# Kernel optimization log

Hardware: AMD Instinct MI355X
Metric: run time of the kernel (lower is better)

Reference implementation:

```python
import jax, jax.numpy as jnp
import numpy as np

B, T, E = 2, 2048, 1024
H, D = 16, 64          # num_heads, head_dim (v_head_dim == head_dim)


def setup_inputs() -> dict:
    key = jax.random.key(0)
    ks = jax.random.split(key, 10)
    s = lambda fan_in: 1.0 / np.sqrt(fan_in)
    inp = {
        "embed": jax.random.normal(ks[0], (B, T, E), dtype=jnp.float32),
        "mask": jax.random.randint(ks[1], (B, T, T), 0, 2) > 0,
        # Linear weights stored as [in, out] (y = x @ W + b)
        "Wq": jax.random.uniform(ks[2], (E, H * D), minval=-s(E), maxval=s(E)),
        "bq": jnp.zeros((H * D,), jnp.float32),
        "Wk": jax.random.uniform(ks[3], (E, H * D), minval=-s(E), maxval=s(E)),
        "bk": jnp.zeros((H * D,), jnp.float32),
        "Wv": jax.random.uniform(ks[4], (E, H * D), minval=-s(E), maxval=s(E)),
        "bv": jnp.zeros((H * D,), jnp.float32),
        "Wz": jax.random.uniform(ks[5], (H * D, E), minval=-s(H * D), maxval=s(H * D)),
        "bz": jnp.zeros((E,), jnp.float32),
    }
    return inp


def reference(embed, mask, Wq, bq, Wk, bk, Wv, bv, Wz, bz):
    # Self-attention: context = embed
    q = (embed @ Wq + bq).reshape(B, T, H, D)   # b t h d
    k = (embed @ Wk + bk).reshape(B, T, H, D)   # b T h d
    v = (embed @ Wv + bv).reshape(B, T, H, D)   # b T h d

    scale = D ** (-0.5)
    score = jnp.einsum('bthd,bThd->bhtT', q, k) * scale   # [b,h,t,T] materialized, as in source
    max_neg = -jnp.finfo(score.dtype).max
    score = jnp.where(mask[:, None, :, :], score, max_neg)
    norm_score = jax.nn.softmax(score, axis=-1)
    z = jnp.einsum('bhtT,bThd->bthd', norm_score, v)      # [b,t,h,d]
    flat_z = z.reshape(B, T, H * D)
    return flat_z @ Wz + bz
```

## Files before the change

### kernel.cpp

```cpp
#include <hip/hip_runtime.h>
#include <hip/hip_bf16.h>


typedef __bf16 bf8_t  __attribute__((ext_vector_type(8)));
typedef __bf16 bf4_t  __attribute__((ext_vector_type(4)));
typedef float  f4_t   __attribute__((ext_vector_type(4)));

constexpr int Bb = 2, Tt = 2048, Hh = 16, Dd = 64;

#define ASYNC16(g, l)                                                        \
    __builtin_amdgcn_global_load_lds(                                        \
        (const __attribute__((address_space(1))) void*)(g),                  \
        (__attribute__((address_space(3))) void*)(l), 16, 0, 0)

#if __has_builtin(__builtin_amdgcn_exp2f)
#define EXP2F(x) __builtin_amdgcn_exp2f(x)
#else
#define EXP2F(x) exp2f(x)
#endif

__global__ __launch_bounds__(256) void prep_kernel(
    const float* __restrict__ embed, const int* __restrict__ mask,
    const float* __restrict__ w0, const float* __restrict__ w1,
    const float* __restrict__ w2, const float* __restrict__ w3,
    __bf16* __restrict__ o0, __bf16* __restrict__ o1,
    __bf16* __restrict__ o2, __bf16* __restrict__ o3,
    __bf16* __restrict__ Eb, unsigned* __restrict__ Mbits)
{
    int z = blockIdx.x;
    if (z < 4096) {
        const float* in; __bf16* out;
        switch (z >> 10) {
            case 0: in = w0; out = o0; break;
            case 1: in = w1; out = o1; break;
            case 2: in = w2; out = o2; break;
            default: in = w3; out = o3; break;
        }
        int rem = z & 1023;
        int bx = (rem & 31) * 32;
        int by = (rem >> 5) * 32;
        __shared__ float t[32][33];
        int x  = threadIdx.x & 31;
        int y0 = threadIdx.x >> 5;
        #pragma unroll
        for (int i = 0; i < 4; i++) {
            int y = y0 + i * 8;
            t[y][x] = in[(size_t)(by + y) * 1024 + bx + x];
        }
        __syncthreads();
        #pragma unroll
        for (int i = 0; i < 4; i++) {
            int y = y0 + i * 8;
            out[(size_t)(bx + y) * 1024 + by + x] = (__bf16)t[x][y];
        }
    } else if (z < 5120) {
        size_t base = (size_t)(z - 4096) * 4096;
        #pragma unroll
        for (int j = 0; j < 4; j++) {
            size_t i = base + j * 1024 + threadIdx.x * 4;
            float4 v = *reinterpret_cast<const float4*>(embed + i);
            bf4_t o = {(__bf16)v.x, (__bf16)v.y, (__bf16)v.z, (__bf16)v.w};
            *reinterpret_cast<bf4_t*>(Eb + i) = o;
        }
    } else {
        size_t g = (size_t)(z - 5120) * 256 + threadIdx.x;
        const int* mp = mask + g * 32;
        unsigned v = 0;
        #pragma unroll
        for (int i = 0; i < 8; i++) {
            int4 m4 = *reinterpret_cast<const int4*>(mp + i * 4);
            if (m4.x) v |= 1u << (i * 4 + 0);
            if (m4.y) v |= 1u << (i * 4 + 1);
            if (m4.z) v |= 1u << (i * 4 + 2);
            if (m4.w) v |= 1u << (i * 4 + 3);
        }
        Mbits[g] = v;
    }
}

template <int TM, typename OutT>
__device__ __forceinline__ void gemm_body(const __bf16* __restrict__ A,
                                          const __bf16* __restrict__ Bt,
                                          const float* __restrict__ bias,
                                          OutT* __restrict__ out,
                                          int mode, float oscale, int bx, int by)
{
    constexpr int NI = TM / 32;
    alignas(16) __shared__ __bf16 As[TM * 64];
    alignas(16) __shared__ __bf16 Bs[128 * 64];

    int tid  = threadIdx.x;
    int lane = tid & 63;
    int quad = lane >> 4;
    int l16  = lane & 15;
    int wave = tid >> 6;
    int wm   = wave >> 1, wn = wave & 1;

    f4_t acc[NI][4];
    #pragma unroll
    for (int i = 0; i < NI; i++)
        #pragma unroll
        for (int j = 0; j < 4; j++)
            acc[i][j] = f4_t{0.f, 0.f, 0.f, 0.f};

    for (int kt = 0; kt < 1024; kt += 64) {
        #pragma unroll
        for (int i = 0; i < TM / 32; i++) {
            int c   = tid + 256 * i;
            int row = c >> 3, j = c & 7;
            ASYNC16(A + (size_t)(by * TM + row) * 1024 + kt + ((j ^ (row & 7)) * 8),
                    &As[c * 8]);
        }
        #pragma unroll
        for (int i = 0; i < 4; i++) {
            int c   = tid + 256 * i;
            int row = c >> 3, j = c & 7;
            ASYNC16(Bt + (size_t)(bx * 128 + row) * 1024 + kt + ((j ^ (row & 7)) * 8),
                    &Bs[c * 8]);
        }
        __syncthreads();

        bf8_t af[2][NI], bfr[2][4];
        #pragma unroll
        for (int c = 0; c < 2; c++) {
            #pragma unroll
            for (int im = 0; im < NI; im++) {
                int row = wm * (TM / 2) + im * 16 + l16;
                af[c][im] = *reinterpret_cast<const bf8_t*>(
                    &As[row * 64 + (((c * 4 + quad) ^ (row & 7)) * 8)]);
            }
            #pragma unroll
            for (int in_ = 0; in_ < 4; in_++) {
                int row = wn * 64 + in_ * 16 + l16;
                bfr[c][in_] = *reinterpret_cast<const bf8_t*>(
                    &Bs[row * 64 + (((c * 4 + quad) ^ (row & 7)) * 8)]);
            }
        }
        #pragma unroll
        for (int c = 0; c < 2; c++)
            #pragma unroll
            for (int im = 0; im < NI; im++)
                #pragma unroll
                for (int in_ = 0; in_ < 4; in_++)
                    acc[im][in_] = __builtin_amdgcn_mfma_f32_16x16x32_bf16(
                        af[c][im], bfr[c][in_], acc[im][in_], 0, 0, 0);
        __syncthreads();
    }

    #pragma unroll
    for (int im = 0; im < NI; im++) {
        #pragma unroll
        for (int in_ = 0; in_ < 4; in_++) {
            int gc  = bx * 128 + wn * 64 + in_ * 16 + l16;
            float bb = bias[gc];
            int gr0 = by * TM + wm * (TM / 2) + im * 16 + quad * 4;
            if (mode == 2) {
                int b = gr0 >> 11, t0 = gr0 & 2047;
                int h = gc >> 6,  d = gc & 63;
                bf4_t ov;
                #pragma unroll
                for (int r = 0; r < 4; r++)
                    ov[r] = (__bf16)(acc[im][in_][r] + bb);
                *reinterpret_cast<bf4_t*>(
                    (__bf16*)out + ((size_t)(b * Hh + h) * Dd + d) * Tt + t0) = ov;
            } else {
                #pragma unroll
                for (int r = 0; r < 4; r++) {
                    int gr  = gr0 + r;
                    float v = (acc[im][in_][r] + bb) * oscale;
                    size_t idx;
                    if (mode == 0) {
                        idx = (size_t)gr * 1024 + gc;
                    } else {
                        int b = gr >> 11, t = gr & 2047;
                        int h = gc >> 6,  d = gc & 63;
                        idx = ((size_t)(b * Hh + h) * Tt + t) * Dd + d;
                    }
                    out[idx] = (OutT)v;
                }
            }
        }
    }
}

__global__ __launch_bounds__(256) void gemm_qkv_kernel(
    const __bf16* __restrict__ A,
    const __bf16* __restrict__ WqT, const __bf16* __restrict__ WkT, const __bf16* __restrict__ WvT,
    const float* __restrict__ bq,  const float* __restrict__ bk,  const float* __restrict__ bv,
    __bf16* __restrict__ Qo, __bf16* __restrict__ Ko, __bf16* __restrict__ Vo)
{
    const __bf16* Bt; const float* bias; __bf16* out; int mode; float sc;
    if      (blockIdx.z == 0) { Bt = WqT; bias = bq; out = Qo; mode = 1; sc = 0.18033688011112042f; }
    else if (blockIdx.z == 1) { Bt = WkT; bias = bk; out = Ko; mode = 1; sc = 1.f; }
    else                      { Bt = WvT; bias = bv; out = Vo; mode = 2; sc = 1.f; }
    gemm_body<128, __bf16>(A, Bt, bias, out, mode, sc, blockIdx.x, blockIdx.y);
}

__global__ __launch_bounds__(256) void gemm_out_kernel(
    const __bf16* __restrict__ A, const __bf16* __restrict__ Bt,
    const float* __restrict__ bias, float* __restrict__ out)
{
    gemm_body<64, float>(A, Bt, bias, out, 0, 1.f, blockIdx.x, blockIdx.y);
}

__global__ __launch_bounds__(512, 4) void flash_kernel(
    const __bf16* __restrict__ Qb, const __bf16* __restrict__ Kb,
    const __bf16* __restrict__ Vb, const unsigned* __restrict__ Mbits,
    __bf16* __restrict__ Zb)
{
    alignas(16) __shared__ __bf16 Ks[2][64 * 64];
    alignas(16) __shared__ __bf16 Vs[2][64 * 64];
    alignas(16) __shared__ __bf16 Ps[8 * 16 * 72];

    int tid  = threadIdx.x;
    int lane = tid & 63;
    int wave = tid >> 6;
    int quad = lane >> 4;
    int l16  = lane & 15;
    int b = blockIdx.z, h = blockIdx.y;
    int bh = b * Hh + h;
    int qrow = blockIdx.x * 128 + wave * 16;

    int srow = tid >> 3, sj = tid & 7;
    const __bf16* kgp = Kb + ((size_t)bh * Tt + srow) * Dd + ((sj ^ (srow & 7)) * 8);
    const __bf16* vgp = Vb + ((size_t)bh * Dd + srow) * Tt + ((sj ^ (srow & 7)) * 8);
    const int sdst = tid * 8;

    bf8_t qf[2];
    #pragma unroll
    for (int c = 0; c < 2; c++)
        qf[c] = *reinterpret_cast<const bf8_t*>(
            Qb + ((size_t)bh * Tt + qrow + l16) * Dd + c * 32 + quad * 8);

    bf8_t ones;
    #pragma unroll
    for (int i = 0; i < 8; i++) ones[i] = (__bf16)1.0f;

    const unsigned* bmp = Mbits + ((size_t)b * Tt + qrow + l16) * 64;

    f4_t lacc = f4_t{0.f, 0.f, 0.f, 0.f};
    f4_t o[4];
    #pragma unroll
    for (int d = 0; d < 4; d++) o[d] = f4_t{0.f, 0.f, 0.f, 0.f};

    __bf16* pw = Ps + wave * 16 * 72;

    bf8_t kreg = *reinterpret_cast<const bf8_t*>(kgp);
    bf8_t vreg = *reinterpret_cast<const bf8_t*>(vgp);
    unsigned long long mreg = *reinterpret_cast<const unsigned long long*>(bmp);

    for (int kt = 0; kt < Tt; kt += 64) {
        int par = (kt >> 6) & 1;
        *reinterpret_cast<bf8_t*>(&Ks[par][sdst]) = kreg;
        *reinterpret_cast<bf8_t*>(&Vs[par][sdst]) = vreg;
        unsigned nib[4];
        #pragma unroll
        for (int n = 0; n < 4; n++)
            nib[n] = (unsigned)(mreg >> (n * 16 + quad * 4)) & 0xFu;
        __syncthreads();

        int ktn = (kt + 64 < Tt) ? kt + 64 : 0;
        kreg = *reinterpret_cast<const bf8_t*>(kgp + (size_t)ktn * Dd);
        vreg = *reinterpret_cast<const bf8_t*>(vgp + ktn);
        mreg = *reinterpret_cast<const unsigned long long*>(bmp + (ktn >> 5));

        f4_t s[4];
        #pragma unroll
        for (int n = 0; n < 4; n++) s[n] = f4_t{0.f, 0.f, 0.f, 0.f};
        __builtin_amdgcn_s_setprio(1);
        #pragma unroll
        for (int c = 0; c < 2; c++)
            #pragma unroll
            for (int n = 0; n < 4; n++) {
                int krow = n * 16 + l16;
                bf8_t kf = *reinterpret_cast<const bf8_t*>(
                    &Ks[par][krow * 64 + (((c * 4 + quad) ^ (krow & 7)) * 8)]);
                s[n] = __builtin_amdgcn_mfma_f32_16x16x32_bf16(kf, qf[c], s[n], 0, 0, 0);
            }
        __builtin_amdgcn_s_setprio(0);

        #pragma unroll
        for (int n = 0; n < 4; n++) {
            bf4_t pv4;
            #pragma unroll
            for (int r = 0; r < 4; r++) {
                float p = (nib[n] & (1u << r)) ? EXP2F(s[n][r]) : 0.f;
                pv4[r] = (__bf16)p;
            }
            *reinterpret_cast<bf4_t*>(&pw[l16 * 72 + n * 16 + quad * 4]) = pv4;
        }

        __builtin_amdgcn_s_setprio(1);
        #pragma unroll
        for (int c = 0; c < 2; c++) {
            bf8_t pf = *reinterpret_cast<const bf8_t*>(
                &pw[l16 * 72 + c * 32 + quad * 8]);
            lacc = __builtin_amdgcn_mfma_f32_16x16x32_bf16(ones, pf, lacc, 0, 0, 0);
            #pragma unroll
            for (int ds = 0; ds < 4; ds++) {
                int vrow = ds * 16 + l16;
                bf8_t vf = *reinterpret_cast<const bf8_t*>(
                    &Vs[par][vrow * 64 + (((c * 4 + quad) ^ (vrow & 7)) * 8)]);
                o[ds] = __builtin_amdgcn_mfma_f32_16x16x32_bf16(vf, pf, o[ds], 0, 0, 0);
            }
        }
        __builtin_amdgcn_s_setprio(0);
    }

    float inv = 1.f / fmaxf(lacc[0], 1e-30f);
    size_t zrow = ((size_t)b * Tt + qrow + l16) * 1024 + h * 64;
    #pragma unroll
    for (int ds = 0; ds < 4; ds++) {
        bf4_t ov;
        #pragma unroll
        for (int r = 0; r < 4; r++) ov[r] = (__bf16)(o[ds][r] * inv);
        *reinterpret_cast<bf4_t*>(Zb + zrow + ds * 16 + quad * 4) = ov;
    }
}

extern "C" void kernel_launch(void* const* d_in, const int* in_sizes, int n_in,
                              void* d_out, int out_size, void* d_ws, size_t ws_size,
                              hipStream_t stream)
{
    (void)in_sizes; (void)n_in; (void)out_size; (void)ws_size;

    const float* embed = (const float*)d_in[0];
    const int*   mask  = (const int*)d_in[1];
    const float* Wq = (const float*)d_in[2];
    const float* bq = (const float*)d_in[3];
    const float* Wk = (const float*)d_in[4];
    const float* bk = (const float*)d_in[5];
    const float* Wv = (const float*)d_in[6];
    const float* bv = (const float*)d_in[7];
    const float* Wz = (const float*)d_in[8];
    const float* bz = (const float*)d_in[9];
    float* out = (float*)d_out;

    char* ws = (char*)d_ws;
    const size_t MB = (size_t)1024 * 1024;
    __bf16*   WqT = (__bf16*)(ws + 0 * MB);
    __bf16*   WkT = (__bf16*)(ws + 2 * MB);
    __bf16*   WvT = (__bf16*)(ws + 4 * MB);
    __bf16*   WzT = (__bf16*)(ws + 6 * MB);
    __bf16*   Eb  = (__bf16*)(ws + 8 * MB);
    __bf16*   Qb  = (__bf16*)(ws + 16 * MB);
    __bf16*   Kb  = (__bf16*)(ws + 24 * MB);
    __bf16*   Vb  = (__bf16*)(ws + 32 * MB);
    __bf16*   Zb  = (__bf16*)(ws + 40 * MB);
    unsigned* Mb  = (unsigned*)(ws + 48 * MB);

    prep_kernel<<<dim3(6144), 256, 0, stream>>>(embed, mask, Wq, Wk, Wv, Wz,
                                                WqT, WkT, WvT, WzT, Eb, Mb);
    gemm_qkv_kernel<<<dim3(8, 32, 3), 256, 0, stream>>>(Eb, WqT, WkT, WvT,
                                                        bq, bk, bv, Qb, Kb, Vb);
    flash_kernel<<<dim3(16, Hh, Bb), 512, 0, stream>>>(Qb, Kb, Vb, Mb, Zb);
    gemm_out_kernel<<<dim3(8, 64, 1), 256, 0, stream>>>(Zb, WzT, bz, out);
}
```

Before: 224.2 us.

## Split each flash query tile's key block across two waves with final reduction

```diff
diff --git a/kernel.cpp b/kernel.cpp
--- a/kernel.cpp
+++ b/kernel.cpp
@@ -203,28 +203,35 @@
     gemm_body<64, float>(A, Bt, bias, out, 0, 1.f, blockIdx.x, blockIdx.y);
 }
 
-__global__ __launch_bounds__(512, 4) void flash_kernel(
+__global__ __launch_bounds__(1024, 8) void flash_kernel(
     const __bf16* __restrict__ Qb, const __bf16* __restrict__ Kb,
     const __bf16* __restrict__ Vb, const unsigned* __restrict__ Mbits,
     __bf16* __restrict__ Zb)
 {
-    alignas(16) __shared__ __bf16 Ks[2][64 * 64];
-    alignas(16) __shared__ __bf16 Vs[2][64 * 64];
-    alignas(16) __shared__ __bf16 Ps[8 * 16 * 72];
+    alignas(16) __shared__ char smem[51200];
+    __bf16* Ks = (__bf16*)smem;
+    __bf16* Vs = (__bf16*)(smem + 16384);
+    __bf16* Ps = (__bf16*)(smem + 32768);
+    float*  fscr = (float*)smem;
 
     int tid  = threadIdx.x;
     int lane = tid & 63;
     int wave = tid >> 6;
+    int s    = wave >> 1;
+    int hk   = wave & 1;
     int quad = lane >> 4;
     int l16  = lane & 15;
     int b = blockIdx.z, h = blockIdx.y;
     int bh = b * Hh + h;
-    int qrow = blockIdx.x * 128 + wave * 16;
-
-    int srow = tid >> 3, sj = tid & 7;
+    int qrow = blockIdx.x * 128 + s * 16;
+
+    int st = tid & 511, srow = st >> 3, sj = st & 7;
+    bool stageK = (wave < 8);
     const __bf16* kgp = Kb + ((size_t)bh * Tt + srow) * Dd + ((sj ^ (srow & 7)) * 8);
     const __bf16* vgp = Vb + ((size_t)bh * Dd + srow) * Tt + ((sj ^ (srow & 7)) * 8);
-    const int sdst = tid * 8;
+    const __bf16* sgp = stageK ? kgp : vgp;
+    const size_t  sstep = stageK ? (size_t)64 * Dd : (size_t)64;
+    __bf16* sdstp = (stageK ? Ks : Vs) + st * 8;
 
     bf8_t qf[2];
     #pragma unroll
@@ -243,78 +250,93 @@
     #pragma unroll
     for (int d = 0; d < 4; d++) o[d] = f4_t{0.f, 0.f, 0.f, 0.f};
 
-    __bf16* pw = Ps + wave * 16 * 72;
-
-    bf8_t kreg = *reinterpret_cast<const bf8_t*>(kgp);
-    bf8_t vreg = *reinterpret_cast<const bf8_t*>(vgp);
+    __bf16* pw = Ps + s * (16 * 72);
+
+    bf8_t sreg = *reinterpret_cast<const bf8_t*>(sgp);
     unsigned long long mreg = *reinterpret_cast<const unsigned long long*>(bmp);
 
     for (int kt = 0; kt < Tt; kt += 64) {
         int par = (kt >> 6) & 1;
-        *reinterpret_cast<bf8_t*>(&Ks[par][sdst]) = kreg;
-        *reinterpret_cast<bf8_t*>(&Vs[par][sdst]) = vreg;
-        unsigned nib[4];
-        #pragma unroll
-        for (int n = 0; n < 4; n++)
-            nib[n] = (unsigned)(mreg >> (n * 16 + quad * 4)) & 0xFu;
+        *reinterpret_cast<bf8_t*>(sdstp + par * 4096) = sreg;
+        unsigned nib0 = (unsigned)(mreg >> (hk * 32 + quad * 4)) & 0xFu;
+        unsigned nib1 = (unsigned)(mreg >> (hk * 32 + 16 + quad * 4)) & 0xFu;
         __syncthreads();
 
         int ktn = (kt + 64 < Tt) ? kt + 64 : 0;
-        kreg = *reinterpret_cast<const bf8_t*>(kgp + (size_t)ktn * Dd);
-        vreg = *reinterpret_cast<const bf8_t*>(vgp + ktn);
+        sreg = *reinterpret_cast<const bf8_t*>(sgp + (size_t)(ktn >> 6) * sstep);
         mreg = *reinterpret_cast<const unsigned long long*>(bmp + (ktn >> 5));
 
-        f4_t s[4];
-        #pragma unroll
-        for (int n = 0; n < 4; n++) s[n] = f4_t{0.f, 0.f, 0.f, 0.f};
+        f4_t sA = f4_t{0.f, 0.f, 0.f, 0.f};
+        f4_t sB = f4_t{0.f, 0.f, 0.f, 0.f};
         __builtin_amdgcn_s_setprio(1);
         #pragma unroll
-        for (int c = 0; c < 2; c++)
-            #pragma unroll
-            for (int n = 0; n < 4; n++) {
-                int krow = n * 16 + l16;
-                bf8_t kf = *reinterpret_cast<const bf8_t*>(
-                    &Ks[par][krow * 64 + (((c * 4 + quad) ^ (krow & 7)) * 8)]);
-                s[n] = __builtin_amdgcn_mfma_f32_16x16x32_bf16(kf, qf[c], s[n], 0, 0, 0);
-            }
+        for (int c = 0; c < 2; c++) {
+            int krow0 = hk * 32 + l16;
+            bf8_t kf0 = *reinterpret_cast<const bf8_t*>(
+                &Ks[par * 4096 + krow0 * 64 + (((c * 4 + quad) ^ (krow0 & 7)) * 8)]);
+            sA = __builtin_amdgcn_mfma_f32_16x16x32_bf16(kf0, qf[c], sA, 0, 0, 0);
+            int krow1 = hk * 32 + 16 + l16;
+            bf8_t kf1 = *reinterpret_cast<const bf8_t*>(
+                &Ks[par * 4096 + krow1 * 64 + (((c * 4 + quad) ^ (krow1 & 7)) * 8)]);
+            sB = __builtin_amdgcn_mfma_f32_16x16x32_bf16(kf1, qf[c], sB, 0, 0, 0);
+        }
         __builtin_amdgcn_s_setprio(0);
 
-        #pragma unroll
-        for (int n = 0; n < 4; n++) {
+        {
             bf4_t pv4;
             #pragma unroll
             for (int r = 0; r < 4; r++) {
-                float p = (nib[n] & (1u << r)) ? EXP2F(s[n][r]) : 0.f;
+                float p = (nib0 & (1u << r)) ? EXP2F(sA[r]) : 0.f;
                 pv4[r] = (__bf16)p;
             }
-            *reinterpret_cast<bf4_t*>(&pw[l16 * 72 + n * 16 + quad * 4]) = pv4;
-        }
-
+            *reinterpret_cast<bf4_t*>(&pw[l16 * 72 + hk * 32 + quad * 4]) = pv4;
+            #pragma unroll
+            for (int r = 0; r < 4; r++) {
+                float p = (nib1 & (1u << r)) ? EXP2F(sB[r]) : 0.f;
+                pv4[r] = (__bf16)p;
+            }
+            *reinterpret_cast<bf4_t*>(&pw[l16 * 72 + hk * 32 + 16 + quad * 4]) = pv4;
+        }
+
+        bf8_t pf = *reinterpret_cast<const bf8_t*>(
+            &pw[l16 * 72 + hk * 32 + quad * 8]);
         __builtin_amdgcn_s_setprio(1);
-        #pragma unroll
-        for (int c = 0; c < 2; c++) {
-            bf8_t pf = *reinterpret_cast<const bf8_t*>(
-                &pw[l16 * 72 + c * 32 + quad * 8]);
-            lacc = __builtin_amdgcn_mfma_f32_16x16x32_bf16(ones, pf, lacc, 0, 0, 0);
-            #pragma unroll
-            for (int ds = 0; ds < 4; ds++) {
-                int vrow = ds * 16 + l16;
-                bf8_t vf = *reinterpret_cast<const bf8_t*>(
-                    &Vs[par][vrow * 64 + (((c * 4 + quad) ^ (vrow & 7)) * 8)]);
-                o[ds] = __builtin_amdgcn_mfma_f32_16x16x32_bf16(vf, pf, o[ds], 0, 0, 0);
-            }
+        lacc = __builtin_amdgcn_mfma_f32_16x16x32_bf16(ones, pf, lacc, 0, 0, 0);
+        #pragma unroll
+        for (int ds = 0; ds < 4; ds++) {
+            int vrow = ds * 16 + l16;
+            bf8_t vf = *reinterpret_cast<const bf8_t*>(
+                &Vs[par * 4096 + vrow * 64 + (((hk * 4 + quad) ^ (vrow & 7)) * 8)]);
+            o[ds] = __builtin_amdgcn_mfma_f32_16x16x32_bf16(vf, pf, o[ds], 0, 0, 0);
         }
         __builtin_amdgcn_s_setprio(0);
     }
 
-    float inv = 1.f / fmaxf(lacc[0], 1e-30f);
-    size_t zrow = ((size_t)b * Tt + qrow + l16) * 1024 + h * 64;
-    #pragma unroll
-    for (int ds = 0; ds < 4; ds++) {
-        bf4_t ov;
-        #pragma unroll
-        for (int r = 0; r < 4; r++) ov[r] = (__bf16)(o[ds][r] * inv);
-        *reinterpret_cast<bf4_t*>(Zb + zrow + ds * 16 + quad * 4) = ov;
+    __syncthreads();
+    float* ws = fscr + s * (64 * 20);
+    if (hk) {
+        #pragma unroll
+        for (int ds = 0; ds < 4; ds++)
+            *reinterpret_cast<f4_t*>(&ws[lane * 20 + ds * 4]) = o[ds];
+        ws[lane * 20 + 16] = lacc[0];
+    }
+    __syncthreads();
+    if (!hk) {
+        #pragma unroll
+        for (int ds = 0; ds < 4; ds++) {
+            f4_t op = *reinterpret_cast<const f4_t*>(&ws[lane * 20 + ds * 4]);
+            o[ds] += op;
+        }
+        float l = lacc[0] + ws[lane * 20 + 16];
+        float inv = 1.f / fmaxf(l, 1e-30f);
+        size_t zrow = ((size_t)b * Tt + qrow + l16) * 1024 + h * 64;
+        #pragma unroll
+        for (int ds = 0; ds < 4; ds++) {
+            bf4_t ov;
+            #pragma unroll
+            for (int r = 0; r < 4; r++) ov[r] = (__bf16)(o[ds][r] * inv);
+            *reinterpret_cast<bf4_t*>(Zb + zrow + ds * 16 + quad * 4) = ov;
+        }
     }
 }
 
@@ -353,6 +375,6 @@
                                                 WqT, WkT, WvT, WzT, Eb, Mb);
     gemm_qkv_kernel<<<dim3(8, 32, 3), 256, 0, stream>>>(Eb, WqT, WkT, WvT,
                                                         bq, bk, bv, Qb, Kb, Vb);
-    flash_kernel<<<dim3(16, Hh, Bb), 512, 0, stream>>>(Qb, Kb, Vb, Mb, Zb);
+    flash_kernel<<<dim3(16, Hh, Bb), 1024, 0, stream>>>(Qb, Kb, Vb, Mb, Zb);
     gemm_out_kernel<<<dim3(8, 64, 1), 256, 0, stream>>>(Zb, WzT, bz, out);
 }
```

Result: slower. 235.4 us (+5.0%).
